# Kernel tuning notes

Measured on AMD Instinct MI355X. Metric: run time of the kernel, lower is better.

The kernel has to match this reference:

```python
import jax
jax.config.update("jax_enable_x64", True)
import jax.numpy as jnp
import numpy as np

CKA_WEIGHT = 0.1


def _group_cka_sum(feats):
    """feats: [F, N, D] float. Returns sum of pairwise CKA over all (i,j) pairs.

    Faithful to CKASR: K = X X^T with zeroed diagonal, unbiased HSIC
    (Song et al. estimator), CKA[i,j] = HSIC(Ki,Kj)/sqrt(HSIC(Ki,Ki)HSIC(Kj,Kj)).
    All pairwise loops are batched into einsums.
    """
    F, N, D = feats.shape
    X = feats.reshape(F, N, D).astype(jnp.float64)
    K = jnp.einsum('fnd,fmd->fnm', X, X)                 # [F,N,N] Gram
    K = K * (1.0 - jnp.eye(N, dtype=K.dtype))            # fill_diagonal_(0)
    # HSIC(Ki, Kj) = 1/(N(N-3)) * ( tr(Ki Kj)
    #   + sum(Ki) sum(Kj) / ((N-1)(N-2))
    #   - 2/(N-2) * <rowsum(Ki), rowsum(Kj)> )
    trKL = jnp.einsum('iab,jab->ij', K, K)               # tr(Ki Kj), K symmetric
    s = jnp.sum(K, axis=(1, 2))                          # [F] total sums
    r = jnp.sum(K, axis=2)                               # [F,N] row sums
    rr = jnp.einsum('ia,ja->ij', r, r)                   # [F,F]
    hsic = (trKL + jnp.outer(s, s) / ((N - 1) * (N - 2))
            - 2.0 * rr / (N - 2)) / (N * (N - 3))        # [F,F]
    d = jnp.sqrt(jnp.diagonal(hsic))                     # [F]
    cka = hsic / (d[:, None] * d[None, :])
    return jnp.sum(cka)


def setup_inputs() -> dict:
    key = jax.random.key(0)
    k1, k2, k3, k4 = jax.random.split(key, 4)
    N, C = 64, 1000
    output = jax.random.normal(k1, (N, C), dtype=jnp.float32)
    target = jax.random.randint(k2, (N,), 0, C, dtype=jnp.int64)
    feats_a = jax.random.normal(k3, (3, N, 65536), dtype=jnp.float32)
    feats_b = jax.random.normal(k4, (4, N, 32768), dtype=jnp.float32)
    return {"output": output, "target": target,
            "feats_a": feats_a, "feats_b": feats_b}


def reference(output, target, feats_a, feats_b):
    N = output.shape[0]
    logp = jax.nn.log_softmax(output.astype(jnp.float32), axis=-1)
    ce = -jnp.mean(logp[jnp.arange(N), target])           # CrossEntropyLoss (mean)
    cka = _group_cka_sum(feats_a) + _group_cka_sum(feats_b)
    loss = ce + CKA_WEIGHT * cka.astype(jnp.float32)
    return (loss, output)
```

## Files before the change

kernel.cpp:

```cpp
#include <hip/hip_runtime.h>
#include <hip/hip_bf16.h>
#include <math.h>

typedef __attribute__((ext_vector_type(8))) short short8;
typedef __attribute__((ext_vector_type(4))) float f32x4;

#define CHUNK_B 16384
#define SLAB_A_F 8388608u
#define SLAB_B_F 4194304u
#define LROW 528

__device__ __forceinline__ unsigned int bf16_rn(float x) {
    unsigned int u = __float_as_uint(x);
    return (u + 0x7FFFu + ((u >> 16) & 1u)) >> 16;
}

__global__ __launch_bounds__(256) void ce_kernel(
    const float* __restrict__ logits, const int* __restrict__ target,
    float* __restrict__ out_copy, float* __restrict__ ce_rows,
    float* __restrict__ K)
{
    const int row = blockIdx.x;
    const float* x = logits + row * 1000;
    const int t = threadIdx.x;
    __shared__ float red[256];

    for (int i = t; i < 448; i += 256) K[row * 448 + i] = 0.f;

    float m = -INFINITY;
    for (int i = t; i < 1000; i += 256) {
        float v = x[i];
        out_copy[row * 1000 + i] = v;
        m = fmaxf(m, v);
    }
    red[t] = m; __syncthreads();
    for (int s = 128; s > 0; s >>= 1) {
        if (t < s) red[t] = fmaxf(red[t], red[t + s]);
        __syncthreads();
    }
    m = red[0];
    __syncthreads();

    float ssum = 0.f;
    for (int i = t; i < 1000; i += 256) ssum += expf(x[i] - m);
    red[t] = ssum; __syncthreads();
    for (int s = 128; s > 0; s >>= 1) {
        if (t < s) red[t] += red[t + s];
        __syncthreads();
    }
    if (t == 0) {
        double lse = (double)m + log((double)red[0]);
        int tg = target[row];
        ce_rows[row] = (float)(-((double)x[tg] - lse));
    }
}

__global__ __launch_bounds__(256) void repack_kernel(
    const float* __restrict__ A, const float* __restrict__ B,
    char* __restrict__ slab, int nfA, int nfB)
{
    __shared__ __align__(16) char lds[64 * LROW];

    const int uA = nfA * 256;
    const int u = blockIdx.x;
    const float* xbase; char* slabF; int D, span;
    if (u < uA) {
        int f = u >> 8; span = u & 255; D = 65536;
        xbase = A + (size_t)f * 64 * D;
        slabF = slab + (size_t)f * SLAB_A_F;
    } else {
        int v = u - uA;
        int f = v >> 7; span = v & 127; D = 32768;
        xbase = B + (size_t)f * 64 * D;
        slabF = slab + (size_t)nfA * SLAB_A_F + (size_t)f * SLAB_B_F;
    }
    const int k0 = span * 256;
    const int wave = threadIdx.x >> 6, lane = threadIdx.x & 63;

    float4 v[16];
#pragma unroll
    for (int i = 0; i < 16; ++i) {
        int row = wave * 16 + i;
        v[i] = *(const float4*)(xbase + (size_t)row * D + k0 + lane * 4);
    }
#pragma unroll
    for (int i = 0; i < 16; ++i) {
        int row = wave * 16 + i;
        uint2 h;
        h.x = bf16_rn(v[i].x) | (bf16_rn(v[i].y) << 16);
        h.y = bf16_rn(v[i].z) | (bf16_rn(v[i].w) << 16);
        *(uint2*)(lds + row * LROW + lane * 8) = h;
    }
    __syncthreads();

    const int m = lane & 15;
#pragma unroll
    for (int cc = 0; cc < 2; ++cc) {
        const int c = span * 2 + cc;
#pragma unroll
        for (int tm = 0; tm < 4; ++tm) {
            int row = tm * 16 + m;
            int kl = cc * 128 + wave * 32 + ((lane >> 4) << 3);
            short8 s = *(const short8*)(lds + row * LROW + kl * 2);
            *(short8*)(slabF + (size_t)c * CHUNK_B + wave * 4096
                       + tm * 1024 + lane * 16) = s;
        }
    }
}

__global__ __launch_bounds__(256) void gram_kernel(
    const char* __restrict__ slab, float* __restrict__ K,
    int nfA, int nfB, int fBase)
{
    __shared__ float kbuf[4096];
    const int blk = blockIdx.x;
    const int f = blk >> 6, local = blk & 63;

    const char* slabF; int c0, nchunk;
    if (f < nfA) {
        slabF = slab + (size_t)f * SLAB_A_F; c0 = local * 8; nchunk = 8;
    } else {
        slabF = slab + (size_t)nfA * SLAB_A_F + (size_t)(f - nfA) * SLAB_B_F;
        c0 = local * 4; nchunk = 4;
    }

    const int t = threadIdx.x;
    const int wave = t >> 6, lane = t & 63;
    const int m = lane & 15, quad = lane >> 4;
    const char* base = slabF + (size_t)c0 * CHUNK_B + wave * 4096 + lane * 16;

    f32x4 acc[4][4];
#pragma unroll
    for (int i = 0; i < 4; ++i)
#pragma unroll
        for (int j = 0; j < 4; ++j) acc[i][j] = (f32x4)0.f;

    short8 cur[4], nxt[4];
#pragma unroll
    for (int tm = 0; tm < 4; ++tm)
        cur[tm] = *(const short8*)(base + tm * 1024);

    for (int ci = 0; ci < nchunk; ++ci) {
        if (ci + 1 < nchunk) {
            const char* nb = base + (size_t)(ci + 1) * CHUNK_B;
#pragma unroll
            for (int tm = 0; tm < 4; ++tm)
                nxt[tm] = *(const short8*)(nb + tm * 1024);
        }
#pragma unroll
        for (int tm = 0; tm < 4; ++tm)
#pragma unroll
            for (int tn = 0; tn < 4; ++tn)
                acc[tm][tn] = __builtin_amdgcn_mfma_f32_16x16x32_bf16(
                    cur[tm], cur[tn], acc[tm][tn], 0, 0, 0);
#pragma unroll
        for (int tm = 0; tm < 4; ++tm) cur[tm] = nxt[tm];
    }

    __syncthreads();
    if (wave == 0) {
#pragma unroll
        for (int tm = 0; tm < 4; ++tm)
#pragma unroll
            for (int tn = 0; tn < 4; ++tn)
#pragma unroll
                for (int r = 0; r < 4; ++r)
                    kbuf[(tm * 16 + quad * 4 + r) * 64 + tn * 16 + m] = acc[tm][tn][r];
    }
    __syncthreads();
    if (wave != 0) {
#pragma unroll
        for (int tm = 0; tm < 4; ++tm)
#pragma unroll
            for (int tn = 0; tn < 4; ++tn)
#pragma unroll
                for (int r = 0; r < 4; ++r)
                    atomicAdd(&kbuf[(tm * 16 + quad * 4 + r) * 64 + tn * 16 + m],
                              acc[tm][tn][r]);
    }
    __syncthreads();

    float* Kf = K + (size_t)(fBase + f) * 4096;
    for (int e = t; e < 4096; e += 256)
        if ((e >> 6) != (e & 63)) atomicAdd(&Kf[e], kbuf[e]);
}

__global__ __launch_bounds__(256) void hsic_kernel(
    const float* __restrict__ K, double* __restrict__ hsic_out)
{
    const int p = blockIdx.x;
    int i, j;
    if (p < 9) { i = p / 3; j = p % 3; }
    else       { int q = p - 9; i = 3 + q / 4; j = 3 + q % 4; }
    const float* Ki = K + i * 4096;
    const float* Kj = K + j * 4096;

    const int t = threadIdx.x;
    const int wave = t >> 6, lane = t & 63;

    __shared__ double wred[4];
    __shared__ double ri[64], rj[64];

    double local = 0.0;
#pragma unroll 4
    for (int e = t; e < 4096; e += 256)
        local += (double)Ki[e] * (double)Kj[e];
    for (int off = 32; off > 0; off >>= 1)
        local += __shfl_down(local, off);
    if (lane == 0) wred[wave] = local;

    const float* M = (wave < 2) ? Ki : Kj;
    double* R = (wave < 2) ? ri : rj;
    const int r0 = (wave & 1) * 32;
    for (int rr = 0; rr < 32; ++rr) {
        int row = r0 + rr;
        double v = (double)M[row * 64 + lane];
        for (int off = 32; off > 0; off >>= 1)
            v += __shfl_down(v, off);
        if (lane == 0) R[row] = v;
    }
    __syncthreads();

    if (t == 0) {
        double tr = wred[0] + wred[1] + wred[2] + wred[3];
        double rr = 0.0, si = 0.0, sj = 0.0;
        for (int n = 0; n < 64; ++n) {
            rr += ri[n] * rj[n];
            si += ri[n];
            sj += rj[n];
        }
        const double N = 64.0;
        const double c1 = (N - 1.0) * (N - 2.0);
        const double c2 = N - 2.0;
        const double c3 = N * (N - 3.0);
        hsic_out[p] = (tr + si * sj / c1 - 2.0 * rr / c2) / c3;
    }
}

__global__ __launch_bounds__(64) void final_kernel(
    const double* __restrict__ hsic, const float* __restrict__ ce_rows,
    float* __restrict__ out_loss)
{
    const int lane = threadIdx.x;
    double cv = (double)ce_rows[lane];
    for (int off = 32; off > 0; off >>= 1)
        cv += __shfl_down(cv, off);
    if (lane != 0) return;
    double ce = cv / 64.0;

    double cka_total = 0.0;
    for (int i = 0; i < 3; ++i)
        for (int j = 0; j < 3; ++j)
            cka_total += hsic[i * 3 + j] / sqrt(hsic[i * 3 + i] * hsic[j * 3 + j]);
    for (int i = 0; i < 4; ++i)
        for (int j = 0; j < 4; ++j)
            cka_total += hsic[9 + i * 4 + j] / sqrt(hsic[9 + i * 4 + i] * hsic[9 + j * 4 + j]);

    out_loss[0] = (float)(ce + 0.1 * cka_total);
}

extern "C" void kernel_launch(void* const* d_in, const int* in_sizes, int n_in,
                              void* d_out, int out_size, void* d_ws, size_t ws_size,
                              hipStream_t stream)
{
    const float* output  = (const float*)d_in[0];
    const int*   target  = (const int*)d_in[1];
    const float* feats_a = (const float*)d_in[2];
    const float* feats_b = (const float*)d_in[3];
    float* out = (float*)d_out;

    char* ws = (char*)d_ws;
    float*  K       = (float*)ws;
    float*  ce_rows = (float*)(ws + 114688);
    double* hsic    = (double*)(ws + 114944);
    char*   slab    = ws + 131072;

    const size_t slabAll = 3 * (size_t)SLAB_A_F + 4 * (size_t)SLAB_B_F;
    const size_t mainNeed = 131072 + slabAll;

    hipLaunchKernelGGL(ce_kernel, dim3(64), dim3(256), 0, stream,
                       output, target, out + 1, ce_rows, K);

    if (ws_size >= mainNeed) {
        hipLaunchKernelGGL(repack_kernel, dim3(1280), dim3(256), 0, stream,
                           feats_a, feats_b, slab, 3, 4);
        hipLaunchKernelGGL(gram_kernel, dim3(448), dim3(256), 0, stream,
                           (const char*)slab, K, 3, 4, 0);
    } else {
        for (int f = 0; f < 7; ++f) {
            if (f < 3) {
                const float* X = feats_a + (size_t)f * 64 * 65536;
                hipLaunchKernelGGL(repack_kernel, dim3(256), dim3(256), 0, stream,
                                   X, (const float*)nullptr, slab, 1, 0);
                hipLaunchKernelGGL(gram_kernel, dim3(64), dim3(256), 0, stream,
                                   (const char*)slab, K, 1, 0, f);
            } else {
                const float* X = feats_b + (size_t)(f - 3) * 64 * 32768;
                hipLaunchKernelGGL(repack_kernel, dim3(128), dim3(256), 0, stream,
                                   (const float*)nullptr, X, slab, 0, 1);
                hipLaunchKernelGGL(gram_kernel, dim3(64), dim3(256), 0, stream,
                                   (const char*)slab, K, 0, 1, f);
            }
        }
    }

    hipLaunchKernelGGL(hsic_kernel, dim3(25), dim3(256), 0, stream, K, hsic);
    hipLaunchKernelGGL(final_kernel, dim3(1), dim3(64), 0, stream,
                       hsic, ce_rows, out);
}
```

Baseline: 187.3 us.

## Fuse CE, HSIC and final kernels; split Gram into more blocks with replicated K

Drops the separate CE kernel: K zeroing moves into the repack kernel, and CE, HSIC and the final reduction merge into one tail kernel that uses a last-block atomic counter. The Gram kernel now gives each block 2 chunks, using 1280 blocks instead of 448, and spreads atomics over 4 replicated K copies to reduce contention. The tail kernel sums the 4 copies. This cuts launch count and improves occupancy in exchange for extra K reads and more atomic traffic overall.

```diff
diff --git a/kernel.cpp b/kernel.cpp
--- a/kernel.cpp
+++ b/kernel.cpp
@@ -9,57 +9,25 @@
 #define SLAB_A_F 8388608u
 #define SLAB_B_F 4194304u
 #define LROW 528
+#define K4S 28672
 
 __device__ __forceinline__ unsigned int bf16_rn(float x) {
     unsigned int u = __float_as_uint(x);
     return (u + 0x7FFFu + ((u >> 16) & 1u)) >> 16;
 }
 
-__global__ __launch_bounds__(256) void ce_kernel(
-    const float* __restrict__ logits, const int* __restrict__ target,
-    float* __restrict__ out_copy, float* __restrict__ ce_rows,
-    float* __restrict__ K)
-{
-    const int row = blockIdx.x;
-    const float* x = logits + row * 1000;
-    const int t = threadIdx.x;
-    __shared__ float red[256];
-
-    for (int i = t; i < 448; i += 256) K[row * 448 + i] = 0.f;
-
-    float m = -INFINITY;
-    for (int i = t; i < 1000; i += 256) {
-        float v = x[i];
-        out_copy[row * 1000 + i] = v;
-        m = fmaxf(m, v);
-    }
-    red[t] = m; __syncthreads();
-    for (int s = 128; s > 0; s >>= 1) {
-        if (t < s) red[t] = fmaxf(red[t], red[t + s]);
-        __syncthreads();
-    }
-    m = red[0];
-    __syncthreads();
-
-    float ssum = 0.f;
-    for (int i = t; i < 1000; i += 256) ssum += expf(x[i] - m);
-    red[t] = ssum; __syncthreads();
-    for (int s = 128; s > 0; s >>= 1) {
-        if (t < s) red[t] += red[t + s];
-        __syncthreads();
-    }
-    if (t == 0) {
-        double lse = (double)m + log((double)red[0]);
-        int tg = target[row];
-        ce_rows[row] = (float)(-((double)x[tg] - lse));
-    }
-}
-
 __global__ __launch_bounds__(256) void repack_kernel(
     const float* __restrict__ A, const float* __restrict__ B,
-    char* __restrict__ slab, int nfA, int nfB)
+    char* __restrict__ slab, int nfA, int nfB,
+    float* __restrict__ K4, int* __restrict__ counter, int zeroK)
 {
     __shared__ __align__(16) char lds[64 * LROW];
+
+    if (zeroK && blockIdx.x < 32) {
+        float* Kz = K4 + blockIdx.x * 3584;
+        for (int i = threadIdx.x; i < 3584; i += 256) Kz[i] = 0.f;
+        if (blockIdx.x == 0 && threadIdx.x == 0) *counter = 0;
+    }
 
     const int uA = nfA * 256;
     const int u = blockIdx.x;
@@ -109,25 +77,27 @@
 }
 
 __global__ __launch_bounds__(256) void gram_kernel(
-    const char* __restrict__ slab, float* __restrict__ K,
-    int nfA, int nfB, int fBase)
+    const char* __restrict__ slab, float* __restrict__ K4,
+    int aChunks, int fOffset)
 {
     __shared__ float kbuf[4096];
     const int blk = blockIdx.x;
-    const int f = blk >> 6, local = blk & 63;
-
-    const char* slabF; int c0, nchunk;
-    if (f < nfA) {
-        slabF = slab + (size_t)f * SLAB_A_F; c0 = local * 8; nchunk = 8;
-    } else {
-        slabF = slab + (size_t)nfA * SLAB_A_F + (size_t)(f - nfA) * SLAB_B_F;
-        c0 = local * 4; nchunk = 4;
-    }
+    const int c0 = blk * 2;
+    const int fl = (c0 < aChunks) ? (c0 >> 9)
+                 : ((aChunks >> 9) + ((c0 - aChunks) >> 8));
+    const int f = fl + fOffset;
 
     const int t = threadIdx.x;
     const int wave = t >> 6, lane = t & 63;
     const int m = lane & 15, quad = lane >> 4;
-    const char* base = slabF + (size_t)c0 * CHUNK_B + wave * 4096 + lane * 16;
+    const char* base = slab + (size_t)c0 * CHUNK_B + wave * 4096 + lane * 16;
+
+    short8 fr[2][4];
+#pragma unroll
+    for (int c = 0; c < 2; ++c)
+#pragma unroll
+        for (int tm = 0; tm < 4; ++tm)
+            fr[c][tm] = *(const short8*)(base + c * CHUNK_B + tm * 1024);
 
     f32x4 acc[4][4];
 #pragma unroll
@@ -135,27 +105,14 @@
 #pragma unroll
         for (int j = 0; j < 4; ++j) acc[i][j] = (f32x4)0.f;
 
-    short8 cur[4], nxt[4];
-#pragma unroll
-    for (int tm = 0; tm < 4; ++tm)
-        cur[tm] = *(const short8*)(base + tm * 1024);
-
-    for (int ci = 0; ci < nchunk; ++ci) {
-        if (ci + 1 < nchunk) {
-            const char* nb = base + (size_t)(ci + 1) * CHUNK_B;
-#pragma unroll
-            for (int tm = 0; tm < 4; ++tm)
-                nxt[tm] = *(const short8*)(nb + tm * 1024);
-        }
+#pragma unroll
+    for (int c = 0; c < 2; ++c)
 #pragma unroll
         for (int tm = 0; tm < 4; ++tm)
 #pragma unroll
             for (int tn = 0; tn < 4; ++tn)
                 acc[tm][tn] = __builtin_amdgcn_mfma_f32_16x16x32_bf16(
-                    cur[tm], cur[tn], acc[tm][tn], 0, 0, 0);
-#pragma unroll
-        for (int tm = 0; tm < 4; ++tm) cur[tm] = nxt[tm];
-    }
+                    fr[c][tm], fr[c][tn], acc[tm][tn], 0, 0, 0);
 
     __syncthreads();
     if (wave == 0) {
@@ -180,83 +137,124 @@
     }
     __syncthreads();
 
-    float* Kf = K + (size_t)(fBase + f) * 4096;
+    float* Kf = K4 + (size_t)(blk & 3) * K4S + (size_t)f * 4096;
     for (int e = t; e < 4096; e += 256)
         if ((e >> 6) != (e & 63)) atomicAdd(&Kf[e], kbuf[e]);
 }
 
-__global__ __launch_bounds__(256) void hsic_kernel(
-    const float* __restrict__ K, double* __restrict__ hsic_out)
+__global__ __launch_bounds__(256) void tail_kernel(
+    const float* __restrict__ K4, const float* __restrict__ logits,
+    const int* __restrict__ target, float* __restrict__ out_copy,
+    float* __restrict__ ce_rows, double* __restrict__ hsic,
+    int* __restrict__ counter, float* __restrict__ out_loss)
 {
     const int p = blockIdx.x;
-    int i, j;
-    if (p < 9) { i = p / 3; j = p % 3; }
-    else       { int q = p - 9; i = 3 + q / 4; j = 3 + q % 4; }
-    const float* Ki = K + i * 4096;
-    const float* Kj = K + j * 4096;
-
     const int t = threadIdx.x;
     const int wave = t >> 6, lane = t & 63;
-
+    __shared__ float red[256];
     __shared__ double wred[4];
     __shared__ double ri[64], rj[64];
-
-    double local = 0.0;
-#pragma unroll 4
-    for (int e = t; e < 4096; e += 256)
-        local += (double)Ki[e] * (double)Kj[e];
-    for (int off = 32; off > 0; off >>= 1)
-        local += __shfl_down(local, off);
-    if (lane == 0) wred[wave] = local;
-
-    const float* M = (wave < 2) ? Ki : Kj;
-    double* R = (wave < 2) ? ri : rj;
-    const int r0 = (wave & 1) * 32;
-    for (int rr = 0; rr < 32; ++rr) {
-        int row = r0 + rr;
-        double v = (double)M[row * 64 + lane];
+    __shared__ int amLast;
+
+    if (p < 25) {
+        int i, j;
+        if (p < 9) { i = p / 3; j = p % 3; }
+        else       { int q = p - 9; i = 3 + q / 4; j = 3 + q % 4; }
+        const float* Ki = K4 + (size_t)i * 4096;
+        const float* Kj = K4 + (size_t)j * 4096;
+
+        double local = 0.0;
+        for (int e = t; e < 4096; e += 256) {
+            double ki = (double)Ki[e] + (double)Ki[K4S + e]
+                      + (double)Ki[2 * K4S + e] + (double)Ki[3 * K4S + e];
+            double kj = (double)Kj[e] + (double)Kj[K4S + e]
+                      + (double)Kj[2 * K4S + e] + (double)Kj[3 * K4S + e];
+            local += ki * kj;
+        }
         for (int off = 32; off > 0; off >>= 1)
-            v += __shfl_down(v, off);
-        if (lane == 0) R[row] = v;
-    }
-    __syncthreads();
+            local += __shfl_down(local, off);
+        if (lane == 0) wred[wave] = local;
+
+        const float* M = (wave < 2) ? Ki : Kj;
+        double* R = (wave < 2) ? ri : rj;
+        const int r0 = (wave & 1) * 32;
+        for (int rr = 0; rr < 32; ++rr) {
+            int row = r0 + rr;
+            int e = row * 64 + lane;
+            double v = (double)M[e] + (double)M[K4S + e]
+                     + (double)M[2 * K4S + e] + (double)M[3 * K4S + e];
+            for (int off = 32; off > 0; off >>= 1)
+                v += __shfl_down(v, off);
+            if (lane == 0) R[row] = v;
+        }
+        __syncthreads();
+
+        if (t == 0) {
+            double tr = wred[0] + wred[1] + wred[2] + wred[3];
+            double rr = 0.0, si = 0.0, sj = 0.0;
+            for (int n = 0; n < 64; ++n) {
+                rr += ri[n] * rj[n];
+                si += ri[n];
+                sj += rj[n];
+            }
+            const double N = 64.0;
+            hsic[p] = (tr + si * sj / ((N - 1.0) * (N - 2.0))
+                       - 2.0 * rr / (N - 2.0)) / (N * (N - 3.0));
+        }
+    } else {
+        const int row = p - 25;
+        const float* x = logits + row * 1000;
+
+        float mx = -INFINITY;
+        for (int i = t; i < 1000; i += 256) {
+            float v = x[i];
+            out_copy[row * 1000 + i] = v;
+            mx = fmaxf(mx, v);
+        }
+        red[t] = mx; __syncthreads();
+        for (int s = 128; s > 0; s >>= 1) {
+            if (t < s) red[t] = fmaxf(red[t], red[t + s]);
+            __syncthreads();
+        }
+        mx = red[0];
+        __syncthreads();
+        float ssum = 0.f;
+        for (int i = t; i < 1000; i += 256) ssum += expf(x[i] - mx);
+        red[t] = ssum; __syncthreads();
+        for (int s = 128; s > 0; s >>= 1) {
+            if (t < s) red[t] += red[t + s];
+            __syncthreads();
+        }
+        if (t == 0) {
+            double lse = (double)mx + log((double)red[0]);
+            int tg = target[row];
+            ce_rows[row] = (float)(-((double)x[tg] - lse));
+        }
+    }
+
+    __threadfence();
+    __syncthreads();
+    if (t == 0) amLast = (atomicAdd(counter, 1) == 88);
+    __syncthreads();
+    if (!amLast) return;
+    __threadfence();
 
     if (t == 0) {
-        double tr = wred[0] + wred[1] + wred[2] + wred[3];
-        double rr = 0.0, si = 0.0, sj = 0.0;
-        for (int n = 0; n < 64; ++n) {
-            rr += ri[n] * rj[n];
-            si += ri[n];
-            sj += rj[n];
-        }
-        const double N = 64.0;
-        const double c1 = (N - 1.0) * (N - 2.0);
-        const double c2 = N - 2.0;
-        const double c3 = N * (N - 3.0);
-        hsic_out[p] = (tr + si * sj / c1 - 2.0 * rr / c2) / c3;
-    }
-}
-
-__global__ __launch_bounds__(64) void final_kernel(
-    const double* __restrict__ hsic, const float* __restrict__ ce_rows,
-    float* __restrict__ out_loss)
-{
-    const int lane = threadIdx.x;
-    double cv = (double)ce_rows[lane];
-    for (int off = 32; off > 0; off >>= 1)
-        cv += __shfl_down(cv, off);
-    if (lane != 0) return;
-    double ce = cv / 64.0;
-
-    double cka_total = 0.0;
-    for (int i = 0; i < 3; ++i)
-        for (int j = 0; j < 3; ++j)
-            cka_total += hsic[i * 3 + j] / sqrt(hsic[i * 3 + i] * hsic[j * 3 + j]);
-    for (int i = 0; i < 4; ++i)
-        for (int j = 0; j < 4; ++j)
-            cka_total += hsic[9 + i * 4 + j] / sqrt(hsic[9 + i * 4 + i] * hsic[9 + j * 4 + j]);
-
-    out_loss[0] = (float)(ce + 0.1 * cka_total);
+        double ce = 0.0;
+        for (int n = 0; n < 64; ++n) ce += (double)ce_rows[n];
+        ce /= 64.0;
+
+        double cka_total = 0.0;
+        for (int i = 0; i < 3; ++i)
+            for (int j = 0; j < 3; ++j)
+                cka_total += hsic[i * 3 + j] / sqrt(hsic[i * 3 + i] * hsic[j * 3 + j]);
+        for (int i = 0; i < 4; ++i)
+            for (int j = 0; j < 4; ++j)
+                cka_total += hsic[9 + i * 4 + j]
+                             / sqrt(hsic[9 + i * 4 + i] * hsic[9 + j * 4 + j]);
+
+        out_loss[0] = (float)(ce + 0.1 * cka_total);
+    }
 }
 
 extern "C" void kernel_launch(void* const* d_in, const int* in_sizes, int n_in,
@@ -270,41 +268,41 @@
     float* out = (float*)d_out;
 
     char* ws = (char*)d_ws;
-    float*  K       = (float*)ws;
-    float*  ce_rows = (float*)(ws + 114688);
-    double* hsic    = (double*)(ws + 114944);
-    char*   slab    = ws + 131072;
+    float*  K4      = (float*)ws;
+    float*  ce_rows = (float*)(ws + 458752);
+    double* hsic    = (double*)(ws + 459008);
+    int*    counter = (int*)(ws + 459264);
+    char*   slab    = ws + 524288;
 
     const size_t slabAll = 3 * (size_t)SLAB_A_F + 4 * (size_t)SLAB_B_F;
-    const size_t mainNeed = 131072 + slabAll;
-
-    hipLaunchKernelGGL(ce_kernel, dim3(64), dim3(256), 0, stream,
-                       output, target, out + 1, ce_rows, K);
+    const size_t mainNeed = 524288 + slabAll;
 
     if (ws_size >= mainNeed) {
         hipLaunchKernelGGL(repack_kernel, dim3(1280), dim3(256), 0, stream,
-                           feats_a, feats_b, slab, 3, 4);
-        hipLaunchKernelGGL(gram_kernel, dim3(448), dim3(256), 0, stream,
-                           (const char*)slab, K, 3, 4, 0);
+                           feats_a, feats_b, slab, 3, 4, K4, counter, 1);
+        hipLaunchKernelGGL(gram_kernel, dim3(1280), dim3(256), 0, stream,
+                           (const char*)slab, K4, 1536, 0);
     } else {
         for (int f = 0; f < 7; ++f) {
             if (f < 3) {
                 const float* X = feats_a + (size_t)f * 64 * 65536;
                 hipLaunchKernelGGL(repack_kernel, dim3(256), dim3(256), 0, stream,
-                                   X, (const float*)nullptr, slab, 1, 0);
-                hipLaunchKernelGGL(gram_kernel, dim3(64), dim3(256), 0, stream,
-                                   (const char*)slab, K, 1, 0, f);
+                                   X, (const float*)nullptr, slab, 1, 0,
+                                   K4, counter, f == 0 ? 1 : 0);
+                hipLaunchKernelGGL(gram_kernel, dim3(256), dim3(256), 0, stream,
+                                   (const char*)slab, K4, 512, f);
             } else {
                 const float* X = feats_b + (size_t)(f - 3) * 64 * 32768;
                 hipLaunchKernelGGL(repack_kernel, dim3(128), dim3(256), 0, stream,
-                                   (const float*)nullptr, X, slab, 0, 1);
-                hipLaunchKernelGGL(gram_kernel, dim3(64), dim3(256), 0, stream,
-                                   (const char*)slab, K, 0, 1, f);
+                                   (const float*)nullptr, X, slab, 0, 1,
+                                   K4, counter, 0);
+                hipLaunchKernelGGL(gram_kernel, dim3(128), dim3(256), 0, stream,
+                                   (const char*)slab, K4, 0, f);
             }
         }
     }
 
-    hipLaunchKernelGGL(hsic_kernel, dim3(25), dim3(256), 0, stream, K, hsic);
-    hipLaunchKernelGGL(final_kernel, dim3(1), dim3(64), 0, stream,
-                       hsic, ce_rows, out);
-}
+    hipLaunchKernelGGL(tail_kernel, dim3(89), dim3(256), 0, stream,
+                       K4, output, target, out + 1, ce_rows, hsic,
+                       counter, out);
+}
```

Result: slower. 240.5 us (+28.4%).
